# Kernel optimization log

Measured on AMD Instinct MI355X. Metric: run time of the kernel, lower is better.

Reference implementation:

```python
import jax, jax.numpy as jnp
import numpy as np
import math

N_HEADS = 4
N_KV_GROUPS = 1
HEAD_DIM = 256
SLIDING_WINDOW = 512
ROPE_BASE = 1000000.0
EPS = 1e-6


def _rmsnorm(x, gamma):
    # normalize over last dim (head_dim), torch nn.RMSNorm semantics
    ms = jnp.mean(jnp.square(x), axis=-1, keepdims=True)
    return x * jax.lax.rsqrt(ms + EPS) * gamma


def _rope_tables(T, head_dim, dtype):
    inv_freq = 1.0 / (ROPE_BASE ** (jnp.arange(0, head_dim, 2, dtype=jnp.float32) / head_dim))
    t = jnp.arange(T, dtype=jnp.float32)
    freqs = jnp.outer(t, inv_freq)          # [T, head_dim/2]
    return jnp.cos(freqs).astype(dtype), jnp.sin(freqs).astype(dtype)


def _apply_rope(x, cos, sin):
    # x: [B, T, H, hd]; cos/sin: [T, hd/2] broadcast as [1, T, 1, hd/2]
    x0 = x[..., 0::2]
    x1 = x[..., 1::2]
    c = cos[None, :, None, :]
    s = sin[None, :, None, :]
    even = x0 * c - x1 * s
    odd = x0 * s + x1 * c
    return jnp.stack((even, odd), axis=-1).reshape(x.shape)


def setup_inputs() -> dict:
    key = jax.random.key(0)
    ks = jax.random.split(key, 5)
    B, T, C = 2, 4096, 1024
    scale = 0.02
    return {
        "x": jax.random.normal(ks[0], (B, T, C), dtype=jnp.float32),
        "Wq": jax.random.normal(ks[1], (C, C), dtype=jnp.float32) * scale,
        "Wk": jax.random.normal(ks[2], (N_KV_GROUPS * HEAD_DIM, C), dtype=jnp.float32) * scale,
        "Wv": jax.random.normal(ks[3], (N_KV_GROUPS * HEAD_DIM, C), dtype=jnp.float32) * scale,
        "Wo": jax.random.normal(ks[4], (C, C), dtype=jnp.float32) * scale,
        "q_gamma": jnp.ones((HEAD_DIM,), dtype=jnp.float32),
        "k_gamma": jnp.ones((HEAD_DIM,), dtype=jnp.float32),
    }


def reference(x, Wq, Wk, Wv, Wo, q_gamma, k_gamma):
    B, T, C = x.shape
    H, G, hd = N_HEADS, N_KV_GROUPS, HEAD_DIM
    rep = H // G

    q = (x @ Wq.T).reshape(B, T, H, hd)
    k = (x @ Wk.T).reshape(B, T, G, hd)
    v = (x @ Wv.T).reshape(B, T, G, hd)

    q = _rmsnorm(q, q_gamma)
    k = _rmsnorm(k, k_gamma)

    cos, sin = _rope_tables(T, hd, q.dtype)
    q = _apply_rope(q, cos, sin)
    k = _apply_rope(k, cos, sin)

    q = q.transpose(0, 2, 1, 3)                 # [B, H, T, hd]
    k = k.transpose(0, 2, 1, 3)                 # [B, G, T, hd]
    v = v.transpose(0, 2, 1, 3)
    k = jnp.repeat(k, rep, axis=1)              # [B, H, T, hd]
    v = jnp.repeat(v, rep, axis=1)

    scores = jnp.einsum("bhqd,bhkd->bhqk", q, k) / math.sqrt(hd)
    i = jnp.arange(T)[:, None]
    j = jnp.arange(T)[None, :]
    allowed = (j <= i) & (j >= i - SLIDING_WINDOW)   # causal sliding window
    scores = jnp.where(allowed, scores, -jnp.inf)
    attn = jax.nn.softmax(scores, axis=-1)
    out = jnp.einsum("bhqk,bhkd->bhqd", attn, v)     # [B, H, T, hd]
    out = out.transpose(0, 2, 1, 3).reshape(B, T, C)
    return out @ Wo.T
```

## Files before the change

### kernel.cpp

```cpp
#include <hip/hip_runtime.h>
#include <cstdint>
#include <cstddef>

#define T_SEQ 4096
#define NB    2
#define CDIM  1024
#define HD    256
#define NH    4

typedef __attribute__((ext_vector_type(8))) __bf16 bf16x8;
typedef __attribute__((ext_vector_type(4))) __bf16 bf16x4;
typedef __attribute__((ext_vector_type(4))) float  floatx4;
typedef __attribute__((ext_vector_type(16))) float f32x16;

__device__ __forceinline__ floatx4 mfma16(bf16x8 a, bf16x8 b, floatx4 c) {
  return __builtin_amdgcn_mfma_f32_16x16x32_bf16(a, b, c, 0, 0, 0);
}
__device__ __forceinline__ f32x16 mfma32(bf16x8 a, bf16x8 b, f32x16 c) {
  return __builtin_amdgcn_mfma_f32_32x32x16_bf16(a, b, c, 0, 0, 0);
}

__device__ __forceinline__ void gl2lds16(const void* g, void* l) {
  __builtin_amdgcn_global_load_lds(
      (__attribute__((address_space(1))) void*)g,
      (__attribute__((address_space(3))) void*)l, 16, 0, 0);
}

__global__ __launch_bounds__(256) void cvt_all(const float* __restrict__ x,
                                               const float* __restrict__ wq,
                                               const float* __restrict__ wk,
                                               const float* __restrict__ wv,
                                               const float* __restrict__ wo,
                                               __bf16* __restrict__ xb,
                                               __bf16* __restrict__ wb,
                                               __bf16* __restrict__ wob) {
  int i = blockIdx.x * 256 + threadIdx.x;
  const float* src;
  __bf16* dst;
  int off;
  if (i < 2097152)      { src = x;  dst = xb;            off = i; }
  else if (i < 2359296) { src = wq; dst = wb;            off = i - 2097152; }
  else if (i < 2424832) { src = wk; dst = wb + 1048576;  off = i - 2359296; }
  else if (i < 2490368) { src = wv; dst = wb + 1310720;  off = i - 2424832; }
  else                  { src = wo; dst = wob;           off = i - 2490368; }
  float4 v = ((const float4*)src)[off];
  bf16x4 o;
  o[0] = (__bf16)v.x; o[1] = (__bf16)v.y; o[2] = (__bf16)v.z; o[3] = (__bf16)v.w;
  *(bf16x4*)&dst[(size_t)off * 4] = o;
}

template <typename OutT>
__global__ __launch_bounds__(256) void gemm_bt(const __bf16* __restrict__ A,
                                               const __bf16* __restrict__ B,
                                               OutT* __restrict__ C,
                                               int M, int N, int K) {
  __shared__ __bf16 As[128 * 64];
  __shared__ __bf16 Bs[128 * 64];
  const int tid  = threadIdx.x;
  const int lane = tid & 63;
  const int wave = tid >> 6;
  const int wm = wave >> 1, wn = wave & 1;
  const int lrow = lane & 15, quad = lane >> 4;
  const int bm = blockIdx.y, bn = blockIdx.x;

  const __bf16* gA = A + (size_t)(bm * 128) * K;
  const __bf16* gB = B + (size_t)(bn * 128) * K;
  const int arow = tid >> 3;
  const int acol = ((tid & 7) ^ ((tid >> 3) & 7)) * 8;
  const int l7 = lrow & 7;

  floatx4 acc[4][4] = {};

  for (int kt = 0; kt < K; kt += 64) {
#pragma unroll
    for (int i = 0; i < 4; ++i)
      gl2lds16(gA + (size_t)(i * 32 + arow) * K + kt + acol, &As[i * 2048 + tid * 8]);
#pragma unroll
    for (int i = 0; i < 4; ++i)
      gl2lds16(gB + (size_t)(i * 32 + arow) * K + kt + acol, &Bs[i * 2048 + tid * 8]);
    __syncthreads();
#pragma unroll
    for (int kk = 0; kk < 2; ++kk) {
      bf16x8 af[4], bfr[4];
#pragma unroll
      for (int mi = 0; mi < 4; ++mi)
        af[mi] = *(const bf16x8*)&As[(wm * 64 + mi * 16 + lrow) * 64 +
                                     ((kk * 4 + quad) ^ l7) * 8];
#pragma unroll
      for (int ni = 0; ni < 4; ++ni)
        bfr[ni] = *(const bf16x8*)&Bs[(wn * 64 + ni * 16 + lrow) * 64 +
                                      ((kk * 4 + quad) ^ l7) * 8];
#pragma unroll
      for (int mi = 0; mi < 4; ++mi)
#pragma unroll
        for (int ni = 0; ni < 4; ++ni)
          acc[mi][ni] = mfma16(af[mi], bfr[ni], acc[mi][ni]);
    }
    __syncthreads();
  }

  const int row0 = bm * 128 + wm * 64;
  const int col0 = bn * 128 + wn * 64;
#pragma unroll
  for (int mi = 0; mi < 4; ++mi)
#pragma unroll
    for (int ni = 0; ni < 4; ++ni)
#pragma unroll
      for (int r = 0; r < 4; ++r) {
        int row = row0 + mi * 16 + quad * 4 + r;
        int col = col0 + ni * 16 + lrow;
        C[(size_t)row * N + col] = (OutT)acc[mi][ni][r];
      }
}

__global__ __launch_bounds__(256) void rmsrope(const __bf16* __restrict__ qkv,
                                               const float* __restrict__ qg,
                                               const float* __restrict__ kg,
                                               __bf16* __restrict__ qr,
                                               __bf16* __restrict__ kr,
                                               __bf16* __restrict__ vt) {
  __shared__ __bf16 Ls[64 * 256];
  if (blockIdx.x >= 5120) {
    const int vb = blockIdx.x - 5120;
    const int b = vb >> 6, tt = vb & 63;
    const int tid = threadIdx.x;
    const __bf16* src = qkv + ((size_t)(b * 4096 + tt * 64)) * 1536 + 1280;
#pragma unroll
    for (int i = 0; i < 8; ++i)
      gl2lds16(src + (size_t)(i * 8 + (tid >> 5)) * 1536 + (tid & 31) * 8,
               &Ls[i * 2048 + tid * 8]);
    __syncthreads();
    __bf16 buf[64];
#pragma unroll
    for (int i = 0; i < 64; ++i) buf[i] = Ls[i * 256 + tid];
    __bf16* dst = vt + ((size_t)(b * 256 + tid)) * T_SEQ + tt * 64;
#pragma unroll
    for (int i = 0; i < 8; ++i)
      *(bf16x8*)&dst[i * 8] = *(const bf16x8*)&buf[i * 8];
    return;
  }

  const int inst = blockIdx.x * 4 + (threadIdx.x >> 6);
  const int lane = threadIdx.x & 63;
  const int rp = inst / 5, which = inst - rp * 5;
  const int row = rp * 2 + (lane >> 5);
  const int hl = lane & 31;
  const int b = row >> 12, t = row & 4095;

  const int srcoff = (which < 4) ? which * 256 : 1024;
  const __bf16* src = qkv + (size_t)row * 1536 + srcoff;
  bf16x8 xv = *(const bf16x8*)&src[hl * 8];

  float xf[8];
  float ss = 0.f;
#pragma unroll
  for (int j = 0; j < 8; ++j) { xf[j] = (float)xv[j]; ss += xf[j] * xf[j]; }
#pragma unroll
  for (int off = 16; off >= 1; off >>= 1) ss += __shfl_xor(ss, off);
  const float rms = rsqrtf(ss * (1.0f / 256.0f) + 1e-6f);

  const float* g = (which < 4) ? qg : kg;
  const float4 gv0 = *(const float4*)&g[hl * 8];
  const float4 gv1 = *(const float4*)&g[hl * 8 + 4];
  float y[8];
  y[0] = xf[0] * rms * gv0.x; y[1] = xf[1] * rms * gv0.y;
  y[2] = xf[2] * rms * gv0.z; y[3] = xf[3] * rms * gv0.w;
  y[4] = xf[4] * rms * gv1.x; y[5] = xf[5] * rms * gv1.y;
  y[6] = xf[6] * rms * gv1.z; y[7] = xf[7] * rms * gv1.w;

  const float c_log2 = -19.931568569324174f / 128.0f;
  bf16x8 ov;
#pragma unroll
  for (int j = 0; j < 4; ++j) {
    const int p = hl * 4 + j;
    const float a = (float)t * exp2f((float)p * c_log2);
    const float sn = __sinf(a), cs = __cosf(a);
    ov[2 * j]     = (__bf16)(y[2 * j] * cs - y[2 * j + 1] * sn);
    ov[2 * j + 1] = (__bf16)(y[2 * j] * sn + y[2 * j + 1] * cs);
  }

  __bf16* dst = (which < 4)
      ? qr + ((size_t)((b * NH + which) * T_SEQ) + t) * 256
      : kr + ((size_t)(b * T_SEQ) + t) * 256;
  *(bf16x8*)&dst[hl * 8] = ov;
}

__global__ __launch_bounds__(256, 1) void attn(const __bf16* __restrict__ qr,
                                               const __bf16* __restrict__ kr,
                                               const __bf16* __restrict__ vt,
                                               __bf16* __restrict__ ao) {
  __shared__ __bf16 Ks[2][64 * 256];
  __shared__ __bf16 Vs[2][256 * 64];

  const int bid = ((blockIdx.x & 7) << 5) | (blockIdx.x >> 3);
  const int qi = bid & 31, h = (bid >> 5) & 3, b = bid >> 7;
  const int tid = threadIdx.x, w = tid >> 6, lane = tid & 63;
  const int l31 = lane & 31, hi = lane >> 5;

  const __bf16* Q = qr + (size_t)((b * NH + h) * T_SEQ) * 256;
  const __bf16* K = kr + (size_t)(b * T_SEQ) * 256;
  const __bf16* V = vt + (size_t)(b * 256) * T_SEQ;

  const int qbase = qi * 128;
  const int qg = qbase + w * 32 + l31;
  const int wt0 = (qi >= 4) ? 2 * qi - 8 : 0;
  const int wt1 = 2 * qi + 1;

  bf16x8 qf[16];
#pragma unroll
  for (int s = 0; s < 16; ++s)
    qf[s] = *(const bf16x8*)&Q[(size_t)qg * 256 + s * 16 + hi * 8];

  bf16x8 onesv;
#pragma unroll
  for (int j = 0; j < 8; ++j) onesv[j] = (__bf16)1.0f;

  f32x16 o[8] = {};
  f32x16 lm = {};

  const float C1 = 0.09016844005556021f;
  const float C2 = 23.083120654223415f;

#define STAGE_KV(WT)                                                          \
  {                                                                           \
    const int wt_ = (WT);                                                     \
    __bf16* kd = Ks[wt_ & 1];                                                 \
    __bf16* vd = Vs[wt_ & 1];                                                 \
    _Pragma("unroll")                                                         \
    for (int i = 0; i < 8; ++i) {                                             \
      const int row = (w * 8 + i) * 2 + hi;                                   \
      const int g = l31 ^ (row & 7);                                          \
      gl2lds16(K + (size_t)(wt_ * 64 + row) * 256 + g * 8,                    \
               kd + (w * 8 + i) * 512 + lane * 8);                            \
    }                                                                         \
    _Pragma("unroll")                                                         \
    for (int i = 0; i < 8; ++i) {                                             \
      const int row = (w * 8 + i) * 8 + (lane >> 3);                          \
      const int g = (lane & 7) ^ (row & 7);                                   \
      gl2lds16(V + (size_t)row * T_SEQ + wt_ * 64 + g * 8,                    \
               vd + (w * 8 + i) * 512 + lane * 8);                            \
    }                                                                         \
  }

  STAGE_KV(wt0);
  asm volatile("s_waitcnt vmcnt(0)\n\ts_barrier" ::: "memory");

  for (int wt = wt0; wt <= wt1; ++wt) {
    if (wt < wt1) STAGE_KV(wt + 1);

    const __bf16* Kb = Ks[wt & 1];
    const __bf16* Vb = Vs[wt & 1];

    f32x16 s0 = {}, s1 = {};
#pragma unroll
    for (int s = 0; s < 16; ++s) {
      const int c = ((s * 2 + hi) ^ (l31 & 7)) * 8;
      bf16x8 kf0 = *(const bf16x8*)&Kb[(l31) * 256 + c];
      bf16x8 kf1 = *(const bf16x8*)&Kb[(32 + l31) * 256 + c];
      s0 = mfma32(kf0, qf[s], s0);
      s1 = mfma32(kf1, qf[s], s1);
    }

    const bool full = (wt <= 2 * qi - 1) && (wt >= 2 * qi - 6);
    float p0[16], p1[16];
#pragma unroll
    for (int r = 0; r < 16; ++r) {
      const int crow = (r & 3) + 8 * (r >> 2) + 4 * hi;
      float v0 = s0[r], v1 = s1[r];
      if (!full) {
        const int k0 = wt * 64 + crow;
        const int k1 = k0 + 32;
        v0 = ((k0 <= qg) && (k0 + 512 >= qg)) ? v0 : -1e30f;
        v1 = ((k1 <= qg) && (k1 + 512 >= qg)) ? v1 : -1e30f;
      }
      p0[r] = exp2f(v0 * C1 - C2);
      p1[r] = exp2f(v1 * C1 - C2);
    }

    bf16x8 pa[2][2];
#pragma unroll
    for (int kt = 0; kt < 2; ++kt) {
      const float* p = kt ? p1 : p0;
#pragma unroll
      for (int kh = 0; kh < 2; ++kh) {
        unsigned X0, X1, Y0, Y1;
        asm("v_cvt_pk_bf16_f32 %0, %1, %2" : "=v"(X0) : "v"(p[kh * 8 + 0]), "v"(p[kh * 8 + 1]));
        asm("v_cvt_pk_bf16_f32 %0, %1, %2" : "=v"(X1) : "v"(p[kh * 8 + 2]), "v"(p[kh * 8 + 3]));
        asm("v_cvt_pk_bf16_f32 %0, %1, %2" : "=v"(Y0) : "v"(p[kh * 8 + 4]), "v"(p[kh * 8 + 5]));
        asm("v_cvt_pk_bf16_f32 %0, %1, %2" : "=v"(Y1) : "v"(p[kh * 8 + 6]), "v"(p[kh * 8 + 7]));
        const unsigned pX0 = __shfl_xor(X0, 32), pX1 = __shfl_xor(X1, 32);
        const unsigned pY0 = __shfl_xor(Y0, 32), pY1 = __shfl_xor(Y1, 32);
        uint4 wv;
        wv.x = hi ? pY0 : X0;
        wv.y = hi ? pY1 : X1;
        wv.z = hi ? Y0 : pX0;
        wv.w = hi ? Y1 : pX1;
        pa[kt][kh] = __builtin_bit_cast(bf16x8, wv);
      }
    }

#pragma unroll
    for (int kt = 0; kt < 2; ++kt)
#pragma unroll
      for (int kh = 0; kh < 2; ++kh)
        lm = mfma32(pa[kt][kh], onesv, lm);

#pragma unroll
    for (int n = 0; n < 8; ++n) {
      const int vrow = (n * 32 + l31) * 64;
#pragma unroll
      for (int kt = 0; kt < 2; ++kt)
#pragma unroll
        for (int kh = 0; kh < 2; ++kh) {
          bf16x8 vf = *(const bf16x8*)&Vb[vrow +
                                          (((kt * 4 + kh * 2 + hi) ^ (l31 & 7)) * 8)];
          o[n] = mfma32(pa[kt][kh], vf, o[n]);
        }
    }

    if (wt < wt1)
      asm volatile("s_waitcnt vmcnt(0) lgkmcnt(0)\n\ts_barrier" ::: "memory");
  }
#undef STAGE_KV

#pragma unroll
  for (int r = 0; r < 16; ++r) {
    const float rl = 1.0f / lm[r];
    const int qrow = qbase + w * 32 + (r & 3) + 8 * (r >> 2) + 4 * hi;
#pragma unroll
    for (int n = 0; n < 8; ++n)
      ao[((size_t)(b * T_SEQ + qrow)) * CDIM + h * 256 + n * 32 + l31] =
          (__bf16)(o[n][r] * rl);
  }
}

extern "C" void kernel_launch(void* const* d_in, const int* in_sizes, int n_in,
                              void* d_out, int out_size, void* d_ws, size_t ws_size,
                              hipStream_t stream) {
  const float* x  = (const float*)d_in[0];
  const float* Wq = (const float*)d_in[1];
  const float* Wk = (const float*)d_in[2];
  const float* Wv = (const float*)d_in[3];
  const float* Wo = (const float*)d_in[4];
  const float* qg = (const float*)d_in[5];
  const float* kg = (const float*)d_in[6];
  float* out = (float*)d_out;

  const size_t M = (size_t)NB * T_SEQ;
  char* ws = (char*)d_ws;
  __bf16* xb  = (__bf16*)ws; ws += M * CDIM * 2;
  __bf16* wb  = (__bf16*)ws; ws += (size_t)1536 * CDIM * 2;
  __bf16* wob = (__bf16*)ws; ws += (size_t)CDIM * CDIM * 2;
  __bf16* qkv = (__bf16*)ws; ws += M * 1536 * 2;
  __bf16* qr  = (__bf16*)ws; ws += M * CDIM * 2;
  __bf16* kr  = (__bf16*)ws; ws += M * HD * 2;
  __bf16* vt  = (__bf16*)ws; ws += M * HD * 2;
  __bf16* ao  = (__bf16*)ws;

  cvt_all<<<10752, 256, 0, stream>>>(x, Wq, Wk, Wv, Wo, xb, wb, wob);

  gemm_bt<__bf16><<<dim3(12, 64), 256, 0, stream>>>(xb, wb, qkv, 8192, 1536, 1024);

  rmsrope<<<5248, 256, 0, stream>>>(qkv, qg, kg, qr, kr, vt);

  attn<<<NB * NH * (T_SEQ / 128), 256, 0, stream>>>(qr, kr, vt, ao);

  gemm_bt<float><<<dim3(8, 64), 256, 0, stream>>>(ao, wob, out, 8192, 1024, 1024);
}
```

Measured before the change: 220.8 us.

## Split each attention KV tile across two wave groups and reduce via LDS

```diff
diff --git a/kernel.cpp b/kernel.cpp
--- a/kernel.cpp
+++ b/kernel.cpp
@@ -185,16 +185,18 @@
   *(bf16x8*)&dst[hl * 8] = ov;
 }
 
-__global__ __launch_bounds__(256, 1) void attn(const __bf16* __restrict__ qr,
+__global__ __launch_bounds__(512, 2) void attn(const __bf16* __restrict__ qr,
                                                const __bf16* __restrict__ kr,
                                                const __bf16* __restrict__ vt,
                                                __bf16* __restrict__ ao) {
   __shared__ __bf16 Ks[2][64 * 256];
   __shared__ __bf16 Vs[2][256 * 64];
+  __shared__ float  Lx[4][1024];
 
   const int bid = ((blockIdx.x & 7) << 5) | (blockIdx.x >> 3);
   const int qi = bid & 31, h = (bid >> 5) & 3, b = bid >> 7;
   const int tid = threadIdx.x, w = tid >> 6, lane = tid & 63;
+  const int qw = w & 3, kw = w >> 2;
   const int l31 = lane & 31, hi = lane >> 5;
 
   const __bf16* Q = qr + (size_t)((b * NH + h) * T_SEQ) * 256;
@@ -202,7 +204,7 @@
   const __bf16* V = vt + (size_t)(b * 256) * T_SEQ;
 
   const int qbase = qi * 128;
-  const int qg = qbase + w * 32 + l31;
+  const int qg = qbase + qw * 32 + l31;
   const int wt0 = (qi >= 4) ? 2 * qi - 8 : 0;
   const int wt1 = 2 * qi + 1;
 
@@ -227,18 +229,18 @@
     __bf16* kd = Ks[wt_ & 1];                                                 \
     __bf16* vd = Vs[wt_ & 1];                                                 \
     _Pragma("unroll")                                                         \
-    for (int i = 0; i < 8; ++i) {                                             \
-      const int row = (w * 8 + i) * 2 + hi;                                   \
-      const int g = l31 ^ (row & 7);                                          \
+    for (int i = 0; i < 4; ++i) {                                             \
+      const int row = i * 16 + (tid >> 5);                                    \
+      const int g = (tid & 31) ^ (row & 31);                                  \
       gl2lds16(K + (size_t)(wt_ * 64 + row) * 256 + g * 8,                    \
-               kd + (w * 8 + i) * 512 + lane * 8);                            \
+               kd + i * 4096 + tid * 8);                                      \
     }                                                                         \
     _Pragma("unroll")                                                         \
-    for (int i = 0; i < 8; ++i) {                                             \
-      const int row = (w * 8 + i) * 8 + (lane >> 3);                          \
-      const int g = (lane & 7) ^ (row & 7);                                   \
+    for (int i = 0; i < 4; ++i) {                                             \
+      const int row = i * 64 + (tid >> 3);                                    \
+      const int g = (tid & 7) ^ (row & 7);                                    \
       gl2lds16(V + (size_t)row * T_SEQ + wt_ * 64 + g * 8,                    \
-               vd + (w * 8 + i) * 512 + lane * 8);                            \
+               vd + i * 4096 + tid * 8);                                      \
     }                                                                         \
   }
 
@@ -251,86 +253,102 @@
     const __bf16* Kb = Ks[wt & 1];
     const __bf16* Vb = Vs[wt & 1];
 
-    f32x16 s0 = {}, s1 = {};
-#pragma unroll
-    for (int s = 0; s < 16; ++s) {
-      const int c = ((s * 2 + hi) ^ (l31 & 7)) * 8;
-      bf16x8 kf0 = *(const bf16x8*)&Kb[(l31) * 256 + c];
-      bf16x8 kf1 = *(const bf16x8*)&Kb[(32 + l31) * 256 + c];
-      s0 = mfma32(kf0, qf[s], s0);
-      s1 = mfma32(kf1, qf[s], s1);
-    }
+    f32x16 s = {};
+    __builtin_amdgcn_s_setprio(1);
+#pragma unroll
+    for (int st = 0; st < 16; ++st) {
+      bf16x8 kf = *(const bf16x8*)&Kb[(kw * 32 + l31) * 256 +
+                                      (((st * 2 + hi) ^ l31) * 8)];
+      s = mfma32(kf, qf[st], s);
+    }
+    __builtin_amdgcn_s_setprio(0);
 
     const bool full = (wt <= 2 * qi - 1) && (wt >= 2 * qi - 6);
-    float p0[16], p1[16];
+    float p[16];
 #pragma unroll
     for (int r = 0; r < 16; ++r) {
       const int crow = (r & 3) + 8 * (r >> 2) + 4 * hi;
-      float v0 = s0[r], v1 = s1[r];
+      float v = s[r];
       if (!full) {
-        const int k0 = wt * 64 + crow;
-        const int k1 = k0 + 32;
-        v0 = ((k0 <= qg) && (k0 + 512 >= qg)) ? v0 : -1e30f;
-        v1 = ((k1 <= qg) && (k1 + 512 >= qg)) ? v1 : -1e30f;
+        const int k = wt * 64 + kw * 32 + crow;
+        v = ((k <= qg) && (k + 512 >= qg)) ? v : -1e30f;
       }
-      p0[r] = exp2f(v0 * C1 - C2);
-      p1[r] = exp2f(v1 * C1 - C2);
-    }
-
-    bf16x8 pa[2][2];
-#pragma unroll
-    for (int kt = 0; kt < 2; ++kt) {
-      const float* p = kt ? p1 : p0;
-#pragma unroll
-      for (int kh = 0; kh < 2; ++kh) {
-        unsigned X0, X1, Y0, Y1;
-        asm("v_cvt_pk_bf16_f32 %0, %1, %2" : "=v"(X0) : "v"(p[kh * 8 + 0]), "v"(p[kh * 8 + 1]));
-        asm("v_cvt_pk_bf16_f32 %0, %1, %2" : "=v"(X1) : "v"(p[kh * 8 + 2]), "v"(p[kh * 8 + 3]));
-        asm("v_cvt_pk_bf16_f32 %0, %1, %2" : "=v"(Y0) : "v"(p[kh * 8 + 4]), "v"(p[kh * 8 + 5]));
-        asm("v_cvt_pk_bf16_f32 %0, %1, %2" : "=v"(Y1) : "v"(p[kh * 8 + 6]), "v"(p[kh * 8 + 7]));
-        const unsigned pX0 = __shfl_xor(X0, 32), pX1 = __shfl_xor(X1, 32);
-        const unsigned pY0 = __shfl_xor(Y0, 32), pY1 = __shfl_xor(Y1, 32);
-        uint4 wv;
-        wv.x = hi ? pY0 : X0;
-        wv.y = hi ? pY1 : X1;
-        wv.z = hi ? Y0 : pX0;
-        wv.w = hi ? Y1 : pX1;
-        pa[kt][kh] = __builtin_bit_cast(bf16x8, wv);
-      }
-    }
-
-#pragma unroll
-    for (int kt = 0; kt < 2; ++kt)
-#pragma unroll
-      for (int kh = 0; kh < 2; ++kh)
-        lm = mfma32(pa[kt][kh], onesv, lm);
-
+      p[r] = exp2f(v * C1 - C2);
+    }
+
+    bf16x8 pa[2];
+#pragma unroll
+    for (int kh = 0; kh < 2; ++kh) {
+      unsigned X0, X1, Y0, Y1;
+      asm("v_cvt_pk_bf16_f32 %0, %1, %2" : "=v"(X0) : "v"(p[kh * 8 + 0]), "v"(p[kh * 8 + 1]));
+      asm("v_cvt_pk_bf16_f32 %0, %1, %2" : "=v"(X1) : "v"(p[kh * 8 + 2]), "v"(p[kh * 8 + 3]));
+      asm("v_cvt_pk_bf16_f32 %0, %1, %2" : "=v"(Y0) : "v"(p[kh * 8 + 4]), "v"(p[kh * 8 + 5]));
+      asm("v_cvt_pk_bf16_f32 %0, %1, %2" : "=v"(Y1) : "v"(p[kh * 8 + 6]), "v"(p[kh * 8 + 7]));
+      const unsigned pX0 = __shfl_xor(X0, 32), pX1 = __shfl_xor(X1, 32);
+      const unsigned pY0 = __shfl_xor(Y0, 32), pY1 = __shfl_xor(Y1, 32);
+      uint4 wv;
+      wv.x = hi ? pY0 : X0;
+      wv.y = hi ? pY1 : X1;
+      wv.z = hi ? Y0 : pX0;
+      wv.w = hi ? Y1 : pX1;
+      pa[kh] = __builtin_bit_cast(bf16x8, wv);
+    }
+
+    __builtin_amdgcn_s_setprio(1);
+    lm = mfma32(pa[0], onesv, lm);
+    lm = mfma32(pa[1], onesv, lm);
 #pragma unroll
     for (int n = 0; n < 8; ++n) {
       const int vrow = (n * 32 + l31) * 64;
 #pragma unroll
-      for (int kt = 0; kt < 2; ++kt)
-#pragma unroll
-        for (int kh = 0; kh < 2; ++kh) {
-          bf16x8 vf = *(const bf16x8*)&Vb[vrow +
-                                          (((kt * 4 + kh * 2 + hi) ^ (l31 & 7)) * 8)];
-          o[n] = mfma32(pa[kt][kh], vf, o[n]);
-        }
-    }
+      for (int kh = 0; kh < 2; ++kh) {
+        bf16x8 vf = *(const bf16x8*)&Vb[vrow +
+                                        (((kw * 4 + kh * 2 + hi) ^ (l31 & 7)) * 8)];
+        o[n] = mfma32(pa[kh], vf, o[n]);
+      }
+    }
+    __builtin_amdgcn_s_setprio(0);
 
     if (wt < wt1)
       asm volatile("s_waitcnt vmcnt(0) lgkmcnt(0)\n\ts_barrier" ::: "memory");
   }
 #undef STAGE_KV
 
-#pragma unroll
-  for (int r = 0; r < 16; ++r) {
-    const float rl = 1.0f / lm[r];
-    const int qrow = qbase + w * 32 + (r & 3) + 8 * (r >> 2) + 4 * hi;
+  asm volatile("s_waitcnt lgkmcnt(0)\n\ts_barrier" ::: "memory");
+
+  float* red  = (qw < 2) ? ((float*)Ks + qw * 8192) : ((float*)Vs + (qw - 2) * 8192);
+  float* lred = Lx[qw];
+
+  if (kw == 1) {
 #pragma unroll
     for (int n = 0; n < 8; ++n)
-      ao[((size_t)(b * T_SEQ + qrow)) * CDIM + h * 256 + n * 32 + l31] =
-          (__bf16)(o[n][r] * rl);
+#pragma unroll
+      for (int r = 0; r < 16; ++r)
+        red[(n * 16 + r) * 64 + lane] = o[n][r];
+#pragma unroll
+    for (int r = 0; r < 16; ++r)
+      lred[r * 64 + lane] = lm[r];
+  }
+  asm volatile("s_waitcnt lgkmcnt(0)\n\ts_barrier" ::: "memory");
+
+  if (kw == 0) {
+#pragma unroll
+    for (int r = 0; r < 16; ++r) lm[r] += lred[r * 64 + lane];
+#pragma unroll
+    for (int n = 0; n < 8; ++n)
+#pragma unroll
+      for (int r = 0; r < 16; ++r)
+        o[n][r] += red[(n * 16 + r) * 64 + lane];
+
+#pragma unroll
+    for (int r = 0; r < 16; ++r) {
+      const float rl = 1.0f / lm[r];
+      const int qrow = qbase + qw * 32 + (r & 3) + 8 * (r >> 2) + 4 * hi;
+#pragma unroll
+      for (int n = 0; n < 8; ++n)
+        ao[((size_t)(b * T_SEQ + qrow)) * CDIM + h * 256 + n * 32 + l31] =
+            (__bf16)(o[n][r] * rl);
+    }
   }
 }
 
@@ -363,7 +381,7 @@
 
   rmsrope<<<5248, 256, 0, stream>>>(qkv, qg, kg, qr, kr, vt);
 
-  attn<<<NB * NH * (T_SEQ / 128), 256, 0, stream>>>(qr, kr, vt, ao);
+  attn<<<NB * NH * (T_SEQ / 128), 512, 0, stream>>>(qr, kr, vt, ao);
 
   gemm_bt<float><<<dim3(8, 64), 256, 0, stream>>>(ao, wob, out, 8192, 1024, 1024);
 }
```

Measured after the change: 233.4 us. 5.7% more time.
